# Kernel optimization log

Measured on AMD Instinct MI355X. Metric: run time of the kernel, lower is better.

Reference implementation:

```python
import jax, jax.numpy as jnp
import numpy as np

DIM = 256
HEADS = 8
NX = NY = 48
RNG = 5
MAX_IDX = (RNG + 1) ** 2  # 36, padding token


def _make_tokens(nx, ny, rng):
    # Half-symmetric tokenization of 2D relative positions (Learnable_rel_pos_embedding.tokenize)
    xm, ym = np.meshgrid(np.arange(nx), np.arange(ny), indexing='ij')
    xm, ym = xm.ravel(), ym.ravel()
    dx = xm[None, :] - xm[:, None]
    dy = ym[None, :] - ym[:, None]
    tok = np.abs(dx) * (rng + 1) + np.abs(dy)
    tok[(np.abs(dx) > rng) | (np.abs(dy) > rng)] = MAX_IDX
    return tok.astype(np.int32)


def setup_inputs() -> dict:
    key = jax.random.key(0)
    ks = jax.random.split(key, 10)
    s = DIM ** -0.5
    x = jax.random.normal(ks[0], (1, DIM, NX, NY), dtype=jnp.float32)
    Wq = jax.random.normal(ks[1], (DIM, DIM), dtype=jnp.float32) * s
    bq = jax.random.normal(ks[2], (DIM,), dtype=jnp.float32) * 0.01
    Wk = jax.random.normal(ks[3], (DIM, DIM), dtype=jnp.float32) * s
    bk = jax.random.normal(ks[4], (DIM,), dtype=jnp.float32) * 0.01
    Wv = jax.random.normal(ks[5], (DIM, DIM), dtype=jnp.float32) * s
    bv = jax.random.normal(ks[6], (DIM,), dtype=jnp.float32) * 0.01
    Wp = jax.random.normal(ks[7], (DIM, DIM), dtype=jnp.float32) * s
    bp = jax.random.normal(ks[8], (DIM,), dtype=jnp.float32) * 0.01
    emb = jax.random.normal(ks[9], (MAX_IDX + 1, HEADS), dtype=jnp.float32) * 0.02
    tokens = jnp.asarray(_make_tokens(NX, NY, RNG))  # (N, N) int32
    return dict(x=x, Wq=Wq, bq=bq, Wk=Wk, bk=bk, Wv=Wv, bv=bv,
                Wp=Wp, bp=bp, emb=emb, tokens=tokens)


def reference(x, Wq, bq, Wk, bk, Wv, bv, Wp, bp, emb, tokens):
    B, C, nx, ny = x.shape
    H = emb.shape[1]
    hd = C // H
    N = nx * ny
    scale = hd ** -0.5

    def conv1x1(W, b, t):
        return (jnp.einsum('oc,bcxy->boxy', W, t) + b[None, :, None, None])

    # Q/K/V as 1x1 convs, split into heads: (B, H, hd, N)
    q = conv1x1(Wq, bq, x).reshape(B, H, hd, N)
    k = conv1x1(Wk, bk, x).reshape(B, H, hd, N)
    v = conv1x1(Wv, bv, x).reshape(B, H, hd, N)

    # attn_method=2: scores = scale*QK^T + relative positional bias
    scores = jnp.einsum('bhdn,bhdm->bhnm', q, k) * scale  # (B, H, N, N)

    # pos_type=5: embedding lookup over half-symmetric relative-position tokens
    pad = emb.shape[0] - 1
    emb_masked = emb.at[pad].set(0.0)  # padding_idx row is zero
    pe = emb_masked[tokens]            # (N, N, H)
    scores = scores + jnp.transpose(pe, (2, 0, 1))[None]

    attn = jax.nn.softmax(scores, axis=-1)
    out = jnp.einsum('bhnm,bhdm->bhdn', attn, v).reshape(B, C, nx, ny)
    out = conv1x1(Wp, bp, out)
    return out
```

## Files before the change

### kernel.cpp

```cpp
#include <hip/hip_runtime.h>

#define NN 2304
#define CC 256
#define HH 8
#define HD 32
#define NYY 48
#define SCALE 0.17677669529663687f

typedef __bf16 bf16_t;
typedef __bf16 bf8v __attribute__((ext_vector_type(8)));
typedef float f4v __attribute__((ext_vector_type(4)));

__device__ __forceinline__ f4v mfma16(bf8v a, bf8v b, f4v c) {
    return __builtin_amdgcn_mfma_f32_16x16x32_bf16(a, b, c, 0, 0, 0);
}

__global__ __launch_bounds__(256) void k_pre(
    const float* __restrict__ x, bf16_t* __restrict__ xT,
    const float* __restrict__ Wq, const float* __restrict__ Wk,
    const float* __restrict__ Wv, const float* __restrict__ Wp,
    bf16_t* __restrict__ Wb) {
    const int b = blockIdx.x;
    const int t = threadIdx.x;
    if (b < 288) {
        __shared__ float tile[64][33];
        const int c0 = (b & 7) * 32;
        const int n0 = (b >> 3) * 64;
        const int n = t & 63, cb = t >> 6;
#pragma unroll
        for (int cc = 0; cc < 8; cc++) {
            int c = cc * 4 + cb;
            tile[n][c] = x[(size_t)(c0 + c) * NN + n0 + n];
        }
        __syncthreads();
        const int c = t & 31, nb = t >> 5;
#pragma unroll
        for (int nn = 0; nn < 8; nn++) {
            int n2 = nn * 8 + nb;
            xT[(size_t)(n0 + n2) * CC + c0 + c] = (bf16_t)tile[n2][c];
        }
    } else {
        const int wb = b - 288;
        const int matid = wb >> 5;
        const float* src = (matid == 0) ? Wq : (matid == 1) ? Wk : (matid == 2) ? Wv : Wp;
        const int base = (wb & 31) * 2048 + t * 8;
        float4 a = *(const float4*)(src + base);
        float4 c = *(const float4*)(src + base + 4);
        bf8v o;
        o[0] = (bf16_t)a.x; o[1] = (bf16_t)a.y; o[2] = (bf16_t)a.z; o[3] = (bf16_t)a.w;
        o[4] = (bf16_t)c.x; o[5] = (bf16_t)c.y; o[6] = (bf16_t)c.z; o[7] = (bf16_t)c.w;
        *(bf8v*)(Wb + (size_t)matid * 65536 + base) = o;
    }
}

__global__ __launch_bounds__(256) void k_proj_qkv(
    const bf16_t* __restrict__ Wb,
    const float* __restrict__ bq, const float* __restrict__ bk,
    const float* __restrict__ bv,
    const bf16_t* __restrict__ xT,
    bf16_t* __restrict__ Qt, bf16_t* __restrict__ Kt, bf16_t* __restrict__ Vd) {
    const int mat = blockIdx.z;
    const bf16_t* W = Wb + (size_t)mat * 65536;
    const float* bias = (mat == 0) ? bq : (mat == 1) ? bk : bv;
    const int n0 = blockIdx.x * 32;
    const int o0 = blockIdx.y * 64;
    const int lane = threadIdx.x & 63;
    const int wave = threadIdx.x >> 6;
    const int l15 = lane & 15;
    const int quad = lane >> 4;
    const int orow = o0 + wave * 16;

    f4v acc0 = {0.f, 0.f, 0.f, 0.f}, acc1 = {0.f, 0.f, 0.f, 0.f};
#pragma unroll
    for (int k0 = 0; k0 < CC; k0 += 32) {
        bf8v af = *(const bf8v*)(W + (size_t)(orow + l15) * CC + k0 + quad * 8);
        bf8v b0 = *(const bf8v*)(xT + (size_t)(n0 + l15) * CC + k0 + quad * 8);
        bf8v b1 = *(const bf8v*)(xT + (size_t)(n0 + 16 + l15) * CC + k0 + quad * 8);
        acc0 = mfma16(af, b0, acc0);
        acc1 = mfma16(af, b1, acc1);
    }

#pragma unroll
    for (int r = 0; r < 4; r++) {
        const int o = orow + quad * 4 + r;
        const float bo = bias[o];
#pragma unroll
        for (int nb = 0; nb < 2; nb++) {
            const int n = n0 + nb * 16 + l15;
            float v = (nb ? acc1[r] : acc0[r]) + bo;
            if (mat == 2) {
                Vd[(size_t)o * NN + n] = (bf16_t)v;
            } else {
                int h = o >> 5, d = o & 31;
                bf16_t* dst = (mat == 0) ? Qt : Kt;
                float vv = (mat == 0) ? v * SCALE : v;
                dst[(size_t)h * NN * HD + (size_t)n * HD + d] = (bf16_t)vv;
            }
        }
    }
}

__global__ __launch_bounds__(256) void k_attn_split(
    const bf16_t* __restrict__ Qt, const bf16_t* __restrict__ Kt,
    const bf16_t* __restrict__ Vd, const float* __restrict__ emb,
    float* __restrict__ pO, float* __restrict__ pl, int L) {
    __shared__ float lds_emb[40];
    __shared__ bf16_t lds_p[4][16 * 32];
    const int h = blockIdx.x & 7;
    const int qt = blockIdx.x >> 3;
    const int sidx = blockIdx.y;
    const int t = threadIdx.x;
    if (t < 37) lds_emb[t] = (t < 36) ? emb[t * HH + h] : 0.0f;
    __syncthreads();

    const int wave = t >> 6, lane = t & 63;
    const int l15 = lane & 15, quad = lane >> 4;
    const int qg0 = qt * 64 + wave * 16;
    const bf16_t* Qh = Qt + (size_t)h * NN * HD;
    const bf16_t* Kh = Kt + (size_t)h * NN * HD;
    const bf16_t* Vh = Vd + (size_t)h * HD * NN;

    const bf8v aq = *(const bf8v*)(Qh + (size_t)(qg0 + l15) * HD + quad * 8);

    int xi[4], yi[4];
#pragma unroll
    for (int r = 0; r < 4; r++) {
        int qi = qg0 + quad * 4 + r;
        xi[r] = qi / NYY;
        yi[r] = qi - xi[r] * NYY;
    }

    f4v o0 = {0.f, 0.f, 0.f, 0.f}, o1 = {0.f, 0.f, 0.f, 0.f};
    const f4v z = {0.f, 0.f, 0.f, 0.f};
    float lsum[4] = {0.f, 0.f, 0.f, 0.f};
    bf16_t* plds = &lds_p[wave][0];

    const int k_begin = sidx * L, k_end = k_begin + L;
    for (int kb = k_begin; kb < k_end; kb += 32) {
        bf8v kf0 = *(const bf8v*)(Kh + (size_t)(kb + l15) * HD + quad * 8);
        bf8v kf1 = *(const bf8v*)(Kh + (size_t)(kb + 16 + l15) * HD + quad * 8);
        bf8v vf0 = *(const bf8v*)(Vh + (size_t)l15 * NN + kb + quad * 8);
        bf8v vf1 = *(const bf8v*)(Vh + (size_t)(16 + l15) * NN + kb + quad * 8);
        f4v s0 = mfma16(aq, kf0, z);
        f4v s1 = mfma16(aq, kf1, z);
#pragma unroll
        for (int cb = 0; cb < 2; cb++) {
            const f4v& s = cb ? s1 : s0;
            int kj = kb + cb * 16 + l15;
            int xj = kj / NYY;
            int yj = kj - xj * NYY;
#pragma unroll
            for (int r = 0; r < 4; r++) {
                int dx = xi[r] - xj; dx = dx < 0 ? -dx : dx;
                int dy = yi[r] - yj; dy = dy < 0 ? -dy : dy;
                int tok = (dx > 5 || dy > 5) ? 36 : dx * 6 + dy;
                float p = __expf(s[r] + lds_emb[tok]);
                lsum[r] += p;
                plds[(quad * 4 + r) * 32 + cb * 16 + l15] = (bf16_t)p;
            }
        }
        bf8v ap = *(const bf8v*)(plds + l15 * 32 + quad * 8);
        o0 = mfma16(ap, vf0, o0);
        o1 = mfma16(ap, vf1, o1);
    }

    float* pO_s = pO + ((size_t)sidx * HH + h) * NN * HD;
    float* pl_s = pl + ((size_t)sidx * HH + h) * NN;
#pragma unroll
    for (int r = 0; r < 4; r++) {
        float v = lsum[r];
#pragma unroll
        for (int m = 1; m < 16; m <<= 1) v += __shfl_xor(v, m, 64);
        int row = qg0 + quad * 4 + r;
        pO_s[(size_t)row * HD + l15] = o0[r];
        pO_s[(size_t)row * HD + 16 + l15] = o1[r];
        if (l15 == 0) pl_s[row] = v;
    }
}

__global__ __launch_bounds__(256) void k_reduce(
    const float* __restrict__ pO, const float* __restrict__ pl,
    bf16_t* __restrict__ Yt, int S) {
    const int e = blockIdx.x * 256 + threadIdx.x;
    const int h = e / (NN * HD);
    const int rem = e - h * (NN * HD);
    const int q = rem >> 5;
    const int d = rem & 31;
    float so = 0.f, sl = 0.f;
    for (int s = 0; s < S; s++) {
        so += pO[((size_t)s * HH + h) * NN * HD + (size_t)q * HD + d];
        sl += pl[((size_t)s * HH + h) * NN + q];
    }
    Yt[(size_t)q * CC + h * HD + d] = (bf16_t)(so / sl);
}

__global__ __launch_bounds__(256) void k_proj_out(
    const bf16_t* __restrict__ Wb, const float* __restrict__ bp,
    const bf16_t* __restrict__ Yt, float* __restrict__ out) {
    const bf16_t* W = Wb + (size_t)3 * 65536;
    const int n0 = blockIdx.x * 32;
    const int o0 = blockIdx.y * 64;
    const int lane = threadIdx.x & 63;
    const int wave = threadIdx.x >> 6;
    const int l15 = lane & 15;
    const int quad = lane >> 4;
    const int orow = o0 + wave * 16;

    f4v acc0 = {0.f, 0.f, 0.f, 0.f}, acc1 = {0.f, 0.f, 0.f, 0.f};
#pragma unroll
    for (int k0 = 0; k0 < CC; k0 += 32) {
        bf8v af = *(const bf8v*)(W + (size_t)(orow + l15) * CC + k0 + quad * 8);
        bf8v b0 = *(const bf8v*)(Yt + (size_t)(n0 + l15) * CC + k0 + quad * 8);
        bf8v b1 = *(const bf8v*)(Yt + (size_t)(n0 + 16 + l15) * CC + k0 + quad * 8);
        acc0 = mfma16(af, b0, acc0);
        acc1 = mfma16(af, b1, acc1);
    }

#pragma unroll
    for (int r = 0; r < 4; r++) {
        const int o = orow + quad * 4 + r;
        const float bo = bp[o];
        out[(size_t)o * NN + n0 + l15] = acc0[r] + bo;
        out[(size_t)o * NN + n0 + 16 + l15] = acc1[r] + bo;
    }
}

extern "C" void kernel_launch(void* const* d_in, const int* in_sizes, int n_in,
                              void* d_out, int out_size, void* d_ws, size_t ws_size,
                              hipStream_t stream) {
    const float* x   = (const float*)d_in[0];
    const float* Wq  = (const float*)d_in[1];
    const float* bq  = (const float*)d_in[2];
    const float* Wk  = (const float*)d_in[3];
    const float* bk  = (const float*)d_in[4];
    const float* Wv  = (const float*)d_in[5];
    const float* bv  = (const float*)d_in[6];
    const float* Wp  = (const float*)d_in[7];
    const float* bp  = (const float*)d_in[8];
    const float* emb = (const float*)d_in[9];
    float* out = (float*)d_out;

    bf16_t* xT = (bf16_t*)d_ws;
    bf16_t* Qt = xT + (size_t)NN * CC;
    bf16_t* Kt = Qt + (size_t)NN * CC;
    bf16_t* Vd = Kt + (size_t)NN * CC;
    bf16_t* Yt = Vd + (size_t)NN * CC;
    bf16_t* Wb = Yt + (size_t)NN * CC;
    float*  pO = (float*)(Wb + (size_t)4 * CC * CC);

    const size_t base_bytes = (size_t)5 * NN * CC * 2 + (size_t)4 * CC * CC * 2;
    const size_t per_split = (size_t)HH * NN * HD * 4 + (size_t)HH * NN * 4;
    int S = 1;
    if (base_bytes + 8 * per_split <= ws_size) S = 8;
    else if (base_bytes + 4 * per_split <= ws_size) S = 4;
    else if (base_bytes + 2 * per_split <= ws_size) S = 2;
    float* pl = pO + (size_t)S * HH * NN * HD;
    const int L = NN / S;

    hipLaunchKernelGGL(k_pre, dim3(288 + 128), dim3(256), 0, stream,
                       x, xT, Wq, Wk, Wv, Wp, Wb);
    hipLaunchKernelGGL(k_proj_qkv, dim3(72, 4, 3), dim3(256), 0, stream,
                       Wb, bq, bk, bv, xT, Qt, Kt, Vd);
    hipLaunchKernelGGL(k_attn_split, dim3(288, S), dim3(256), 0, stream,
                       Qt, Kt, Vd, emb, pO, pl, L);
    hipLaunchKernelGGL(k_reduce, dim3((HH * NN * HD) / 256), dim3(256), 0, stream,
                       pO, pl, Yt, S);
    hipLaunchKernelGGL(k_proj_out, dim3(72, 4), dim3(256), 0, stream, Wb, bp, Yt, out);
}
```

Before: 151.0 us.

## Fuse all stages into one persistent kernel with grid barriers and skip far bias

Merges the five kernels (prep, QKV projection, split attention, reduce, output projection) into one persistent kernel of 512 blocks that loop over work items, separated by atomic-counter grid barriers. This is meant to remove launch overhead and inter-kernel gaps. Attention tiles whose key rows lie more than 5 grid rows from the query rows now skip the per-element token computation and LDS bias lookup, because the padding embedding is zero there. Risks: the barrier requires all 512 blocks to be co-resident, which could deadlock otherwise. Splits are fixed at 8 with no workspace-size check.

```diff
diff --git a/kernel.cpp b/kernel.cpp
--- a/kernel.cpp
+++ b/kernel.cpp
@@ -6,6 +6,8 @@
 #define HD 32
 #define NYY 48
 #define SCALE 0.17677669529663687f
+#define SPLITS 8
+#define GRID 512
 
 typedef __bf16 bf16_t;
 typedef __bf16 bf8v __attribute__((ext_vector_type(8)));
@@ -15,213 +17,241 @@
     return __builtin_amdgcn_mfma_f32_16x16x32_bf16(a, b, c, 0, 0, 0);
 }
 
-__global__ __launch_bounds__(256) void k_pre(
-    const float* __restrict__ x, bf16_t* __restrict__ xT,
-    const float* __restrict__ Wq, const float* __restrict__ Wk,
-    const float* __restrict__ Wv, const float* __restrict__ Wp,
-    bf16_t* __restrict__ Wb) {
-    const int b = blockIdx.x;
+__device__ __forceinline__ void gbar(int* cnt, int target) {
+    __syncthreads();
+    if (threadIdx.x == 0) {
+        __threadfence();
+        __hip_atomic_fetch_add(cnt, 1, __ATOMIC_RELEASE, __HIP_MEMORY_SCOPE_AGENT);
+        while (__hip_atomic_load(cnt, __ATOMIC_ACQUIRE, __HIP_MEMORY_SCOPE_AGENT) < target) {
+            __builtin_amdgcn_s_sleep(8);
+        }
+        __threadfence();
+    }
+    __syncthreads();
+}
+
+__global__ __launch_bounds__(256, 2) void k_fused(
+    const float* __restrict__ x,
+    const float* __restrict__ Wq, const float* __restrict__ bq,
+    const float* __restrict__ Wk, const float* __restrict__ bk,
+    const float* __restrict__ Wv, const float* __restrict__ bv,
+    const float* __restrict__ Wp, const float* __restrict__ bp,
+    const float* __restrict__ emb,
+    bf16_t* __restrict__ xT, bf16_t* __restrict__ Qt, bf16_t* __restrict__ Kt,
+    bf16_t* __restrict__ Vd, bf16_t* __restrict__ Yt, bf16_t* __restrict__ Wb,
+    float* __restrict__ pO, float* __restrict__ pl, float* __restrict__ out,
+    int* __restrict__ bar)
+{
     const int t = threadIdx.x;
-    if (b < 288) {
-        __shared__ float tile[64][33];
-        const int c0 = (b & 7) * 32;
-        const int n0 = (b >> 3) * 64;
-        const int n = t & 63, cb = t >> 6;
-#pragma unroll
-        for (int cc = 0; cc < 8; cc++) {
-            int c = cc * 4 + cb;
-            tile[n][c] = x[(size_t)(c0 + c) * NN + n0 + n];
-        }
-        __syncthreads();
-        const int c = t & 31, nb = t >> 5;
-#pragma unroll
-        for (int nn = 0; nn < 8; nn++) {
-            int n2 = nn * 8 + nb;
-            xT[(size_t)(n0 + n2) * CC + c0 + c] = (bf16_t)tile[n2][c];
-        }
-    } else {
-        const int wb = b - 288;
-        const int matid = wb >> 5;
-        const float* src = (matid == 0) ? Wq : (matid == 1) ? Wk : (matid == 2) ? Wv : Wp;
-        const int base = (wb & 31) * 2048 + t * 8;
-        float4 a = *(const float4*)(src + base);
-        float4 c = *(const float4*)(src + base + 4);
-        bf8v o;
-        o[0] = (bf16_t)a.x; o[1] = (bf16_t)a.y; o[2] = (bf16_t)a.z; o[3] = (bf16_t)a.w;
-        o[4] = (bf16_t)c.x; o[5] = (bf16_t)c.y; o[6] = (bf16_t)c.z; o[7] = (bf16_t)c.w;
-        *(bf8v*)(Wb + (size_t)matid * 65536 + base) = o;
-    }
-}
-
-__global__ __launch_bounds__(256) void k_proj_qkv(
-    const bf16_t* __restrict__ Wb,
-    const float* __restrict__ bq, const float* __restrict__ bk,
-    const float* __restrict__ bv,
-    const bf16_t* __restrict__ xT,
-    bf16_t* __restrict__ Qt, bf16_t* __restrict__ Kt, bf16_t* __restrict__ Vd) {
-    const int mat = blockIdx.z;
-    const bf16_t* W = Wb + (size_t)mat * 65536;
-    const float* bias = (mat == 0) ? bq : (mat == 1) ? bk : bv;
-    const int n0 = blockIdx.x * 32;
-    const int o0 = blockIdx.y * 64;
-    const int lane = threadIdx.x & 63;
-    const int wave = threadIdx.x >> 6;
-    const int l15 = lane & 15;
-    const int quad = lane >> 4;
-    const int orow = o0 + wave * 16;
-
-    f4v acc0 = {0.f, 0.f, 0.f, 0.f}, acc1 = {0.f, 0.f, 0.f, 0.f};
-#pragma unroll
-    for (int k0 = 0; k0 < CC; k0 += 32) {
-        bf8v af = *(const bf8v*)(W + (size_t)(orow + l15) * CC + k0 + quad * 8);
-        bf8v b0 = *(const bf8v*)(xT + (size_t)(n0 + l15) * CC + k0 + quad * 8);
-        bf8v b1 = *(const bf8v*)(xT + (size_t)(n0 + 16 + l15) * CC + k0 + quad * 8);
-        acc0 = mfma16(af, b0, acc0);
-        acc1 = mfma16(af, b1, acc1);
-    }
-
-#pragma unroll
-    for (int r = 0; r < 4; r++) {
-        const int o = orow + quad * 4 + r;
-        const float bo = bias[o];
-#pragma unroll
-        for (int nb = 0; nb < 2; nb++) {
-            const int n = n0 + nb * 16 + l15;
-            float v = (nb ? acc1[r] : acc0[r]) + bo;
-            if (mat == 2) {
-                Vd[(size_t)o * NN + n] = (bf16_t)v;
-            } else {
-                int h = o >> 5, d = o & 31;
-                bf16_t* dst = (mat == 0) ? Qt : Kt;
-                float vv = (mat == 0) ? v * SCALE : v;
-                dst[(size_t)h * NN * HD + (size_t)n * HD + d] = (bf16_t)vv;
-            }
-        }
-    }
-}
-
-__global__ __launch_bounds__(256) void k_attn_split(
-    const bf16_t* __restrict__ Qt, const bf16_t* __restrict__ Kt,
-    const bf16_t* __restrict__ Vd, const float* __restrict__ emb,
-    float* __restrict__ pO, float* __restrict__ pl, int L) {
-    __shared__ float lds_emb[40];
-    __shared__ bf16_t lds_p[4][16 * 32];
-    const int h = blockIdx.x & 7;
-    const int qt = blockIdx.x >> 3;
-    const int sidx = blockIdx.y;
-    const int t = threadIdx.x;
-    if (t < 37) lds_emb[t] = (t < 36) ? emb[t * HH + h] : 0.0f;
-    __syncthreads();
-
     const int wave = t >> 6, lane = t & 63;
     const int l15 = lane & 15, quad = lane >> 4;
-    const int qg0 = qt * 64 + wave * 16;
-    const bf16_t* Qh = Qt + (size_t)h * NN * HD;
-    const bf16_t* Kh = Kt + (size_t)h * NN * HD;
-    const bf16_t* Vh = Vd + (size_t)h * HD * NN;
-
-    const bf8v aq = *(const bf8v*)(Qh + (size_t)(qg0 + l15) * HD + quad * 8);
-
-    int xi[4], yi[4];
-#pragma unroll
-    for (int r = 0; r < 4; r++) {
-        int qi = qg0 + quad * 4 + r;
-        xi[r] = qi / NYY;
-        yi[r] = qi - xi[r] * NYY;
-    }
-
-    f4v o0 = {0.f, 0.f, 0.f, 0.f}, o1 = {0.f, 0.f, 0.f, 0.f};
-    const f4v z = {0.f, 0.f, 0.f, 0.f};
-    float lsum[4] = {0.f, 0.f, 0.f, 0.f};
-    bf16_t* plds = &lds_p[wave][0];
-
-    const int k_begin = sidx * L, k_end = k_begin + L;
-    for (int kb = k_begin; kb < k_end; kb += 32) {
-        bf8v kf0 = *(const bf8v*)(Kh + (size_t)(kb + l15) * HD + quad * 8);
-        bf8v kf1 = *(const bf8v*)(Kh + (size_t)(kb + 16 + l15) * HD + quad * 8);
-        bf8v vf0 = *(const bf8v*)(Vh + (size_t)l15 * NN + kb + quad * 8);
-        bf8v vf1 = *(const bf8v*)(Vh + (size_t)(16 + l15) * NN + kb + quad * 8);
-        f4v s0 = mfma16(aq, kf0, z);
-        f4v s1 = mfma16(aq, kf1, z);
-#pragma unroll
-        for (int cb = 0; cb < 2; cb++) {
-            const f4v& s = cb ? s1 : s0;
-            int kj = kb + cb * 16 + l15;
-            int xj = kj / NYY;
-            int yj = kj - xj * NYY;
+    __shared__ float smem[2112];
+
+    {
+        const int b = blockIdx.x;
+        if (b < 288) {
+            float (*tile)[33] = (float (*)[33])smem;
+            const int c0 = (b & 7) * 32;
+            const int n0 = (b >> 3) * 64;
+            const int n = t & 63, cb = t >> 6;
+#pragma unroll
+            for (int cc = 0; cc < 8; cc++) {
+                int c = cc * 4 + cb;
+                tile[n][c] = x[(size_t)(c0 + c) * NN + n0 + n];
+            }
+            __syncthreads();
+            const int c2 = t & 31, nb2 = t >> 5;
+#pragma unroll
+            for (int nn = 0; nn < 8; nn++) {
+                int n2 = nn * 8 + nb2;
+                xT[(size_t)(n0 + n2) * CC + c0 + c2] = (bf16_t)tile[n2][c2];
+            }
+        } else if (b < 416) {
+            const int wb = b - 288;
+            const int matid = wb >> 5;
+            const float* src = (matid == 0) ? Wq : (matid == 1) ? Wk : (matid == 2) ? Wv : Wp;
+            const int base = (wb & 31) * 2048 + t * 8;
+            float4 a = *(const float4*)(src + base);
+            float4 c = *(const float4*)(src + base + 4);
+            bf8v o;
+            o[0] = (bf16_t)a.x; o[1] = (bf16_t)a.y; o[2] = (bf16_t)a.z; o[3] = (bf16_t)a.w;
+            o[4] = (bf16_t)c.x; o[5] = (bf16_t)c.y; o[6] = (bf16_t)c.z; o[7] = (bf16_t)c.w;
+            *(bf8v*)(Wb + (size_t)matid * 65536 + base) = o;
+        }
+    }
+    gbar(bar, 1 * GRID);
+
+    for (int u = blockIdx.x; u < 864; u += GRID) {
+        const int nb = u % 72;
+        const int rest = u / 72;
+        const int ob = rest & 3;
+        const int mat = rest >> 2;
+        const bf16_t* W = Wb + (size_t)mat * 65536;
+        const float* bias = (mat == 0) ? bq : (mat == 1) ? bk : bv;
+        const int n0 = nb * 32;
+        const int orow = ob * 64 + wave * 16;
+
+        f4v acc0 = {0.f, 0.f, 0.f, 0.f}, acc1 = {0.f, 0.f, 0.f, 0.f};
+#pragma unroll
+        for (int k0 = 0; k0 < CC; k0 += 32) {
+            bf8v af = *(const bf8v*)(W + (size_t)(orow + l15) * CC + k0 + quad * 8);
+            bf8v b0 = *(const bf8v*)(xT + (size_t)(n0 + l15) * CC + k0 + quad * 8);
+            bf8v b1 = *(const bf8v*)(xT + (size_t)(n0 + 16 + l15) * CC + k0 + quad * 8);
+            acc0 = mfma16(af, b0, acc0);
+            acc1 = mfma16(af, b1, acc1);
+        }
+#pragma unroll
+        for (int r = 0; r < 4; r++) {
+            const int o = orow + quad * 4 + r;
+            const float bo = bias[o];
+#pragma unroll
+            for (int nb2 = 0; nb2 < 2; nb2++) {
+                const int n = n0 + nb2 * 16 + l15;
+                float v = (nb2 ? acc1[r] : acc0[r]) + bo;
+                if (mat == 2) {
+                    Vd[(size_t)o * NN + n] = (bf16_t)v;
+                } else {
+                    int h = o >> 5, d = o & 31;
+                    bf16_t* dst = (mat == 0) ? Qt : Kt;
+                    float vv = (mat == 0) ? v * SCALE : v;
+                    dst[(size_t)h * NN * HD + (size_t)n * HD + d] = (bf16_t)vv;
+                }
+            }
+        }
+    }
+    gbar(bar, 2 * GRID);
+
+    {
+        float* lds_emb = smem;
+        bf16_t* plds = (bf16_t*)(smem + 64) + wave * 512;
+        const int L = NN / SPLITS;
+        const f4v z = {0.f, 0.f, 0.f, 0.f};
+        for (int u = blockIdx.x; u < 288 * SPLITS; u += GRID) {
+            const int bx = u % 288;
+            const int sidx = u / 288;
+            const int h = bx & 7;
+            const int qt = bx >> 3;
+            __syncthreads();
+            if (t < 37) lds_emb[t] = (t < 36) ? emb[t * HH + h] : 0.0f;
+            __syncthreads();
+
+            const int qg0 = qt * 64 + wave * 16;
+            const bf16_t* Qh = Qt + (size_t)h * NN * HD;
+            const bf16_t* Kh = Kt + (size_t)h * NN * HD;
+            const bf16_t* Vh = Vd + (size_t)h * HD * NN;
+            const bf8v aq = *(const bf8v*)(Qh + (size_t)(qg0 + l15) * HD + quad * 8);
+
+            int xi[4], yi[4];
 #pragma unroll
             for (int r = 0; r < 4; r++) {
-                int dx = xi[r] - xj; dx = dx < 0 ? -dx : dx;
-                int dy = yi[r] - yj; dy = dy < 0 ? -dy : dy;
-                int tok = (dx > 5 || dy > 5) ? 36 : dx * 6 + dy;
-                float p = __expf(s[r] + lds_emb[tok]);
-                lsum[r] += p;
-                plds[(quad * 4 + r) * 32 + cb * 16 + l15] = (bf16_t)p;
-            }
-        }
-        bf8v ap = *(const bf8v*)(plds + l15 * 32 + quad * 8);
-        o0 = mfma16(ap, vf0, o0);
-        o1 = mfma16(ap, vf1, o1);
-    }
-
-    float* pO_s = pO + ((size_t)sidx * HH + h) * NN * HD;
-    float* pl_s = pl + ((size_t)sidx * HH + h) * NN;
-#pragma unroll
-    for (int r = 0; r < 4; r++) {
-        float v = lsum[r];
-#pragma unroll
-        for (int m = 1; m < 16; m <<= 1) v += __shfl_xor(v, m, 64);
-        int row = qg0 + quad * 4 + r;
-        pO_s[(size_t)row * HD + l15] = o0[r];
-        pO_s[(size_t)row * HD + 16 + l15] = o1[r];
-        if (l15 == 0) pl_s[row] = v;
-    }
-}
-
-__global__ __launch_bounds__(256) void k_reduce(
-    const float* __restrict__ pO, const float* __restrict__ pl,
-    bf16_t* __restrict__ Yt, int S) {
-    const int e = blockIdx.x * 256 + threadIdx.x;
-    const int h = e / (NN * HD);
-    const int rem = e - h * (NN * HD);
-    const int q = rem >> 5;
-    const int d = rem & 31;
-    float so = 0.f, sl = 0.f;
-    for (int s = 0; s < S; s++) {
-        so += pO[((size_t)s * HH + h) * NN * HD + (size_t)q * HD + d];
-        sl += pl[((size_t)s * HH + h) * NN + q];
-    }
-    Yt[(size_t)q * CC + h * HD + d] = (bf16_t)(so / sl);
-}
-
-__global__ __launch_bounds__(256) void k_proj_out(
-    const bf16_t* __restrict__ Wb, const float* __restrict__ bp,
-    const bf16_t* __restrict__ Yt, float* __restrict__ out) {
-    const bf16_t* W = Wb + (size_t)3 * 65536;
-    const int n0 = blockIdx.x * 32;
-    const int o0 = blockIdx.y * 64;
-    const int lane = threadIdx.x & 63;
-    const int wave = threadIdx.x >> 6;
-    const int l15 = lane & 15;
-    const int quad = lane >> 4;
-    const int orow = o0 + wave * 16;
-
-    f4v acc0 = {0.f, 0.f, 0.f, 0.f}, acc1 = {0.f, 0.f, 0.f, 0.f};
-#pragma unroll
-    for (int k0 = 0; k0 < CC; k0 += 32) {
-        bf8v af = *(const bf8v*)(W + (size_t)(orow + l15) * CC + k0 + quad * 8);
-        bf8v b0 = *(const bf8v*)(Yt + (size_t)(n0 + l15) * CC + k0 + quad * 8);
-        bf8v b1 = *(const bf8v*)(Yt + (size_t)(n0 + 16 + l15) * CC + k0 + quad * 8);
-        acc0 = mfma16(af, b0, acc0);
-        acc1 = mfma16(af, b1, acc1);
-    }
-
-#pragma unroll
-    for (int r = 0; r < 4; r++) {
-        const int o = orow + quad * 4 + r;
-        const float bo = bp[o];
-        out[(size_t)o * NN + n0 + l15] = acc0[r] + bo;
-        out[(size_t)o * NN + n0 + 16 + l15] = acc1[r] + bo;
+                int qi = qg0 + quad * 4 + r;
+                xi[r] = qi / NYY;
+                yi[r] = qi - xi[r] * NYY;
+            }
+            const int xi_lo = qg0 / NYY;
+            const int xi_hi = (qg0 + 15) / NYY;
+
+            f4v o0 = z, o1 = z;
+            float lsum[4] = {0.f, 0.f, 0.f, 0.f};
+
+            const int k_begin = sidx * L, k_end = k_begin + L;
+            for (int kb = k_begin; kb < k_end; kb += 32) {
+                bf8v kf0 = *(const bf8v*)(Kh + (size_t)(kb + l15) * HD + quad * 8);
+                bf8v kf1 = *(const bf8v*)(Kh + (size_t)(kb + 16 + l15) * HD + quad * 8);
+                bf8v vf0 = *(const bf8v*)(Vh + (size_t)l15 * NN + kb + quad * 8);
+                bf8v vf1 = *(const bf8v*)(Vh + (size_t)(16 + l15) * NN + kb + quad * 8);
+                f4v s0 = mfma16(aq, kf0, z);
+                f4v s1 = mfma16(aq, kf1, z);
+
+                const int xj_lo = kb / NYY;
+                const int xj_hi = (kb + 31) / NYY;
+                if (xj_lo > xi_hi + 5 || xj_hi + 5 < xi_lo) {
+#pragma unroll
+                    for (int cb = 0; cb < 2; cb++) {
+                        const f4v& s = cb ? s1 : s0;
+#pragma unroll
+                        for (int r = 0; r < 4; r++) {
+                            float p = __expf(s[r]);
+                            lsum[r] += p;
+                            plds[(quad * 4 + r) * 32 + cb * 16 + l15] = (bf16_t)p;
+                        }
+                    }
+                } else {
+#pragma unroll
+                    for (int cb = 0; cb < 2; cb++) {
+                        const f4v& s = cb ? s1 : s0;
+                        int kj = kb + cb * 16 + l15;
+                        int xj = kj / NYY;
+                        int yj = kj - xj * NYY;
+#pragma unroll
+                        for (int r = 0; r < 4; r++) {
+                            int dx = xi[r] - xj; dx = dx < 0 ? -dx : dx;
+                            int dy = yi[r] - yj; dy = dy < 0 ? -dy : dy;
+                            int tok = (dx > 5 || dy > 5) ? 36 : dx * 6 + dy;
+                            float p = __expf(s[r] + lds_emb[tok]);
+                            lsum[r] += p;
+                            plds[(quad * 4 + r) * 32 + cb * 16 + l15] = (bf16_t)p;
+                        }
+                    }
+                }
+                bf8v ap = *(const bf8v*)(plds + l15 * 32 + quad * 8);
+                o0 = mfma16(ap, vf0, o0);
+                o1 = mfma16(ap, vf1, o1);
+            }
+
+            float* pO_s = pO + ((size_t)sidx * HH + h) * NN * HD;
+            float* pl_s = pl + ((size_t)sidx * HH + h) * NN;
+#pragma unroll
+            for (int r = 0; r < 4; r++) {
+                float v = lsum[r];
+#pragma unroll
+                for (int m = 1; m < 16; m <<= 1) v += __shfl_xor(v, m, 64);
+                int row = qg0 + quad * 4 + r;
+                pO_s[(size_t)row * HD + l15] = o0[r];
+                pO_s[(size_t)row * HD + 16 + l15] = o1[r];
+                if (l15 == 0) pl_s[row] = v;
+            }
+        }
+    }
+    gbar(bar, 3 * GRID);
+
+    for (int u = blockIdx.x; u < (HH * NN * HD) / 256; u += GRID) {
+        const int e = u * 256 + t;
+        const int h = e / (NN * HD);
+        const int rem = e - h * (NN * HD);
+        const int q = rem >> 5;
+        const int d = rem & 31;
+        float so = 0.f, sl = 0.f;
+#pragma unroll
+        for (int s = 0; s < SPLITS; s++) {
+            so += pO[((size_t)s * HH + h) * NN * HD + (size_t)q * HD + d];
+            sl += pl[((size_t)s * HH + h) * NN + q];
+        }
+        Yt[(size_t)q * CC + h * HD + d] = (bf16_t)(so / sl);
+    }
+    gbar(bar, 4 * GRID);
+
+    for (int u = blockIdx.x; u < 288; u += GRID) {
+        const int n0 = (u % 72) * 32;
+        const int orow = (u / 72) * 64 + wave * 16;
+        const bf16_t* W = Wb + (size_t)3 * 65536;
+
+        f4v acc0 = {0.f, 0.f, 0.f, 0.f}, acc1 = {0.f, 0.f, 0.f, 0.f};
+#pragma unroll
+        for (int k0 = 0; k0 < CC; k0 += 32) {
+            bf8v af = *(const bf8v*)(W + (size_t)(orow + l15) * CC + k0 + quad * 8);
+            bf8v b0 = *(const bf8v*)(Yt + (size_t)(n0 + l15) * CC + k0 + quad * 8);
+            bf8v b1 = *(const bf8v*)(Yt + (size_t)(n0 + 16 + l15) * CC + k0 + quad * 8);
+            acc0 = mfma16(af, b0, acc0);
+            acc1 = mfma16(af, b1, acc1);
+        }
+#pragma unroll
+        for (int r = 0; r < 4; r++) {
+            const int o = orow + quad * 4 + r;
+            const float bo = bp[o];
+            out[(size_t)o * NN + n0 + l15] = acc0[r] + bo;
+            out[(size_t)o * NN + n0 + 16 + l15] = acc1[r] + bo;
+        }
     }
 }
 
@@ -247,23 +277,12 @@
     bf16_t* Yt = Vd + (size_t)NN * CC;
     bf16_t* Wb = Yt + (size_t)NN * CC;
     float*  pO = (float*)(Wb + (size_t)4 * CC * CC);
-
-    const size_t base_bytes = (size_t)5 * NN * CC * 2 + (size_t)4 * CC * CC * 2;
-    const size_t per_split = (size_t)HH * NN * HD * 4 + (size_t)HH * NN * 4;
-    int S = 1;
-    if (base_bytes + 8 * per_split <= ws_size) S = 8;
-    else if (base_bytes + 4 * per_split <= ws_size) S = 4;
-    else if (base_bytes + 2 * per_split <= ws_size) S = 2;
-    float* pl = pO + (size_t)S * HH * NN * HD;
-    const int L = NN / S;
-
-    hipLaunchKernelGGL(k_pre, dim3(288 + 128), dim3(256), 0, stream,
-                       x, xT, Wq, Wk, Wv, Wp, Wb);
-    hipLaunchKernelGGL(k_proj_qkv, dim3(72, 4, 3), dim3(256), 0, stream,
-                       Wb, bq, bk, bv, xT, Qt, Kt, Vd);
-    hipLaunchKernelGGL(k_attn_split, dim3(288, S), dim3(256), 0, stream,
-                       Qt, Kt, Vd, emb, pO, pl, L);
-    hipLaunchKernelGGL(k_reduce, dim3((HH * NN * HD) / 256), dim3(256), 0, stream,
-                       pO, pl, Yt, S);
-    hipLaunchKernelGGL(k_proj_out, dim3(72, 4), dim3(256), 0, stream, Wb, bp, Yt, out);
-}
+    float*  pl = pO + (size_t)SPLITS * HH * NN * HD;
+    size_t bar_off = ((size_t)((char*)(pl + (size_t)SPLITS * HH * NN) - (char*)d_ws) + 255) & ~(size_t)255;
+    int* bar = (int*)((char*)d_ws + bar_off);
+
+    hipMemsetAsync(bar, 0, 64, stream);
+    hipLaunchKernelGGL(k_fused, dim3(GRID), dim3(256), 0, stream,
+                       x, Wq, bq, Wk, bk, Wv, bv, Wp, bp, emb,
+                       xT, Qt, Kt, Vd, Yt, Wb, pO, pl, out, bar);
+}
```

Result: slower. 436.2 us (+188.8%).

## Split key range across waves in-block, reduce in LDS, skip far-tile bias

Applied to the files above, without the earlier changes.

Replaces the grid-level key split (partials written to global memory, then a separate reduce kernel) with an in-block split: each block handles 16 queries of one head, its four waves each cover a quarter of the keys, and the partial outputs and sums are combined in shared memory before Yt is written. This removes the fp32 partial-buffer traffic and one kernel launch. A tile-level check also skips the token and bias computation when a key tile lies outside the relative-position window. The trade-off is that each wave now loads its own K/V with no reuse across queries inside the block, so K/V reads from L2 grow roughly fourfold.

```diff
diff --git a/kernel.cpp b/kernel.cpp
--- a/kernel.cpp
+++ b/kernel.cpp
@@ -100,22 +100,24 @@
     }
 }
 
-__global__ __launch_bounds__(256) void k_attn_split(
+__global__ __launch_bounds__(256, 4) void k_attn(
     const bf16_t* __restrict__ Qt, const bf16_t* __restrict__ Kt,
     const bf16_t* __restrict__ Vd, const float* __restrict__ emb,
-    float* __restrict__ pO, float* __restrict__ pl, int L) {
+    bf16_t* __restrict__ Yt) {
     __shared__ float lds_emb[40];
+    __shared__ float red[4][16][33];
+    __shared__ float reds[4][16];
     __shared__ bf16_t lds_p[4][16 * 32];
-    const int h = blockIdx.x & 7;
-    const int qt = blockIdx.x >> 3;
-    const int sidx = blockIdx.y;
+    const int b = blockIdx.x;
+    const int h = b & 7;
+    const int qt = b >> 3;
     const int t = threadIdx.x;
     if (t < 37) lds_emb[t] = (t < 36) ? emb[t * HH + h] : 0.0f;
     __syncthreads();
 
     const int wave = t >> 6, lane = t & 63;
     const int l15 = lane & 15, quad = lane >> 4;
-    const int qg0 = qt * 64 + wave * 16;
+    const int qg0 = qt * 16;
     const bf16_t* Qh = Qt + (size_t)h * NN * HD;
     const bf16_t* Kh = Kt + (size_t)h * NN * HD;
     const bf16_t* Vh = Vd + (size_t)h * HD * NN;
@@ -129,13 +131,15 @@
         xi[r] = qi / NYY;
         yi[r] = qi - xi[r] * NYY;
     }
+    const int xi_lo = qg0 / NYY;
+    const int xi_hi = (qg0 + 15) / NYY;
 
     f4v o0 = {0.f, 0.f, 0.f, 0.f}, o1 = {0.f, 0.f, 0.f, 0.f};
     const f4v z = {0.f, 0.f, 0.f, 0.f};
     float lsum[4] = {0.f, 0.f, 0.f, 0.f};
     bf16_t* plds = &lds_p[wave][0];
 
-    const int k_begin = sidx * L, k_end = k_begin + L;
+    const int k_begin = wave * (NN / 4), k_end = k_begin + NN / 4;
     for (int kb = k_begin; kb < k_end; kb += 32) {
         bf8v kf0 = *(const bf8v*)(Kh + (size_t)(kb + l15) * HD + quad * 8);
         bf8v kf1 = *(const bf8v*)(Kh + (size_t)(kb + 16 + l15) * HD + quad * 8);
@@ -143,20 +147,36 @@
         bf8v vf1 = *(const bf8v*)(Vh + (size_t)(16 + l15) * NN + kb + quad * 8);
         f4v s0 = mfma16(aq, kf0, z);
         f4v s1 = mfma16(aq, kf1, z);
-#pragma unroll
-        for (int cb = 0; cb < 2; cb++) {
-            const f4v& s = cb ? s1 : s0;
-            int kj = kb + cb * 16 + l15;
-            int xj = kj / NYY;
-            int yj = kj - xj * NYY;
-#pragma unroll
-            for (int r = 0; r < 4; r++) {
-                int dx = xi[r] - xj; dx = dx < 0 ? -dx : dx;
-                int dy = yi[r] - yj; dy = dy < 0 ? -dy : dy;
-                int tok = (dx > 5 || dy > 5) ? 36 : dx * 6 + dy;
-                float p = __expf(s[r] + lds_emb[tok]);
-                lsum[r] += p;
-                plds[(quad * 4 + r) * 32 + cb * 16 + l15] = (bf16_t)p;
+
+        const int xj_lo = kb / NYY;
+        const int xj_hi = (kb + 31) / NYY;
+        if (xj_lo > xi_hi + 5 || xj_hi + 5 < xi_lo) {
+#pragma unroll
+            for (int cb = 0; cb < 2; cb++) {
+                const f4v& s = cb ? s1 : s0;
+#pragma unroll
+                for (int r = 0; r < 4; r++) {
+                    float p = __expf(s[r]);
+                    lsum[r] += p;
+                    plds[(quad * 4 + r) * 32 + cb * 16 + l15] = (bf16_t)p;
+                }
+            }
+        } else {
+#pragma unroll
+            for (int cb = 0; cb < 2; cb++) {
+                const f4v& s = cb ? s1 : s0;
+                int kj = kb + cb * 16 + l15;
+                int xj = kj / NYY;
+                int yj = kj - xj * NYY;
+#pragma unroll
+                for (int r = 0; r < 4; r++) {
+                    int dx = xi[r] - xj; dx = dx < 0 ? -dx : dx;
+                    int dy = yi[r] - yj; dy = dy < 0 ? -dy : dy;
+                    int tok = (dx > 5 || dy > 5) ? 36 : dx * 6 + dy;
+                    float p = __expf(s[r] + lds_emb[tok]);
+                    lsum[r] += p;
+                    plds[(quad * 4 + r) * 32 + cb * 16 + l15] = (bf16_t)p;
+                }
             }
         }
         bf8v ap = *(const bf8v*)(plds + l15 * 32 + quad * 8);
@@ -164,34 +184,26 @@
         o1 = mfma16(ap, vf1, o1);
     }
 
-    float* pO_s = pO + ((size_t)sidx * HH + h) * NN * HD;
-    float* pl_s = pl + ((size_t)sidx * HH + h) * NN;
 #pragma unroll
     for (int r = 0; r < 4; r++) {
         float v = lsum[r];
 #pragma unroll
         for (int m = 1; m < 16; m <<= 1) v += __shfl_xor(v, m, 64);
-        int row = qg0 + quad * 4 + r;
-        pO_s[(size_t)row * HD + l15] = o0[r];
-        pO_s[(size_t)row * HD + 16 + l15] = o1[r];
-        if (l15 == 0) pl_s[row] = v;
-    }
-}
-
-__global__ __launch_bounds__(256) void k_reduce(
-    const float* __restrict__ pO, const float* __restrict__ pl,
-    bf16_t* __restrict__ Yt, int S) {
-    const int e = blockIdx.x * 256 + threadIdx.x;
-    const int h = e / (NN * HD);
-    const int rem = e - h * (NN * HD);
-    const int q = rem >> 5;
-    const int d = rem & 31;
-    float so = 0.f, sl = 0.f;
-    for (int s = 0; s < S; s++) {
-        so += pO[((size_t)s * HH + h) * NN * HD + (size_t)q * HD + d];
-        sl += pl[((size_t)s * HH + h) * NN + q];
-    }
-    Yt[(size_t)q * CC + h * HD + d] = (bf16_t)(so / sl);
+        const int row = quad * 4 + r;
+        red[wave][row][l15] = o0[r];
+        red[wave][row][16 + l15] = o1[r];
+        if (l15 == 0) reds[wave][row] = v;
+    }
+    __syncthreads();
+
+#pragma unroll
+    for (int e = t; e < 512; e += 256) {
+        const int row = e >> 5;
+        const int d = e & 31;
+        float so = red[0][row][d] + red[1][row][d] + red[2][row][d] + red[3][row][d];
+        float sl = reds[0][row] + reds[1][row] + reds[2][row] + reds[3][row];
+        Yt[(size_t)(qg0 + row) * CC + h * HD + d] = (bf16_t)(so / sl);
+    }
 }
 
 __global__ __launch_bounds__(256) void k_proj_out(
@@ -246,24 +258,12 @@
     bf16_t* Vd = Kt + (size_t)NN * CC;
     bf16_t* Yt = Vd + (size_t)NN * CC;
     bf16_t* Wb = Yt + (size_t)NN * CC;
-    float*  pO = (float*)(Wb + (size_t)4 * CC * CC);
-
-    const size_t base_bytes = (size_t)5 * NN * CC * 2 + (size_t)4 * CC * CC * 2;
-    const size_t per_split = (size_t)HH * NN * HD * 4 + (size_t)HH * NN * 4;
-    int S = 1;
-    if (base_bytes + 8 * per_split <= ws_size) S = 8;
-    else if (base_bytes + 4 * per_split <= ws_size) S = 4;
-    else if (base_bytes + 2 * per_split <= ws_size) S = 2;
-    float* pl = pO + (size_t)S * HH * NN * HD;
-    const int L = NN / S;
 
     hipLaunchKernelGGL(k_pre, dim3(288 + 128), dim3(256), 0, stream,
                        x, xT, Wq, Wk, Wv, Wp, Wb);
     hipLaunchKernelGGL(k_proj_qkv, dim3(72, 4, 3), dim3(256), 0, stream,
                        Wb, bq, bk, bv, xT, Qt, Kt, Vd);
-    hipLaunchKernelGGL(k_attn_split, dim3(288, S), dim3(256), 0, stream,
-                       Qt, Kt, Vd, emb, pO, pl, L);
-    hipLaunchKernelGGL(k_reduce, dim3((HH * NN * HD) / 256), dim3(256), 0, stream,
-                       pO, pl, Yt, S);
+    hipLaunchKernelGGL(k_attn, dim3(1152), dim3(256), 0, stream,
+                       Qt, Kt, Vd, emb, Yt);
     hipLaunchKernelGGL(k_proj_out, dim3(72, 4), dim3(256), 0, stream, Wb, bp, Yt, out);
 }
```

Result: faster. 141.9 us (-6.0%).
